# Performance work log

Hardware: AMD Instinct MI355X
Metric: run time of the kernel (lower is better)

Reference implementation:

```python
import jax, jax.numpy as jnp
import numpy as np

B, T, D = 64, 128, 1024
H = 8                       # attention heads
C, S, M = 1000, 5, 10       # num_classes, max_stages, mem_size


def layernorm(x, g, b, eps=1e-5):
    mu = jnp.mean(x, axis=-1, keepdims=True)
    var = jnp.var(x, axis=-1, keepdims=True)
    return (x - mu) / jnp.sqrt(var + eps) * g + b


def linear(x, w, b):
    return x @ w.T + b


def lstm_layer(xin, Wih, Whh, bih, bhh):
    # PyTorch gate order: i, f, g, o
    def step(carry, xt):
        h, c = carry
        gates = xt @ Wih.T + bih + h @ Whh.T + bhh
        i, f, g, o = jnp.split(gates, 4, axis=-1)
        c = jax.nn.sigmoid(f) * c + jax.nn.sigmoid(i) * jnp.tanh(g)
        h = jax.nn.sigmoid(o) * jnp.tanh(c)
        return (h, c), h
    z = jnp.zeros((xin.shape[0], Wih.shape[0] // 4), xin.dtype)
    (hF, _), ys = jax.lax.scan(step, (z, z), jnp.swapaxes(xin, 0, 1))
    return jnp.swapaxes(ys, 0, 1), hF


def setup_inputs() -> dict:
    key = jax.random.key(0)
    ks = iter(jax.random.split(key, 64))

    def w(shape, s=0.02):
        return jax.random.normal(next(ks), shape, jnp.float32) * s

    inp = {
        "x": jax.random.normal(next(ks), (B, T, D), jnp.float32),
        "current_stage": jax.random.randint(next(ks), (B, T), 0, S),
        "class_ids": jax.random.randint(next(ks), (B,), 0, C),
        # stage_encoder: Linear(2,64) -> LN -> ReLU -> Linear(64,D) -> LN
        "enc_w1": w((64, 2)), "enc_b1": jnp.zeros((64,)),
        "enc_g1": jnp.ones((64,)), "enc_bb1": jnp.zeros((64,)),
        "enc_w2": w((D, 64)), "enc_b2": jnp.zeros((D,)),
        "enc_g2": jnp.ones((D,)), "enc_bb2": jnp.zeros((D,)),
        # MultiheadAttention in/out projections
        "qkv_w": w((3 * D, D)), "qkv_b": jnp.zeros((3 * D,)),
        "out_w": w((D, D)), "out_b": jnp.zeros((D,)),
        "norm_g": jnp.ones((D,)), "norm_b": jnp.zeros((D,)),
        # 2-layer LSTM
        "Wih0": w((4 * D, D)), "Whh0": w((4 * D, D)),
        "bih0": jnp.zeros((4 * D,)), "bhh0": jnp.zeros((4 * D,)),
        "Wih1": w((4 * D, D)), "Whh1": w((4 * D, D)),
        "bih1": jnp.zeros((4 * D,)), "bhh1": jnp.zeros((4 * D,)),
        # stage_head
        "head_w1": w((D // 2, D)), "head_b1": jnp.zeros((D // 2,)),
        "head_g": jnp.ones((D // 2,)), "head_bb": jnp.zeros((D // 2,)),
        "head_w2": w((S, D // 2)), "head_b2": jnp.zeros((S,)),
        # GlobalFusion gate
        "gate_w1": w((D, 2 * D)), "gate_b1": jnp.zeros((D,)),
        "gate_w2": w((D, D)), "gate_b2": jnp.zeros((D,)),
        # memory bank buffers
        "memory_features": jnp.zeros((C, S, M, D), jnp.float32),
        "memory_counts": jnp.zeros((C, S), jnp.int32),
    }
    return inp


def reference(x, current_stage, class_ids,
              enc_w1, enc_b1, enc_g1, enc_bb1, enc_w2, enc_b2, enc_g2, enc_bb2,
              qkv_w, qkv_b, out_w, out_b, norm_g, norm_b,
              Wih0, Whh0, bih0, bhh0, Wih1, Whh1, bih1, bhh1,
              head_w1, head_b1, head_g, head_bb, head_w2, head_b2,
              gate_w1, gate_b1, gate_w2, gate_b2,
              memory_features, memory_counts):
    Bx, Tx, Dx = x.shape
    # position + stage encoding
    pos = jnp.broadcast_to(jnp.arange(Tx, dtype=jnp.float32), (Bx, Tx))
    ps = jnp.stack([pos, current_stage.astype(jnp.float32)], axis=-1)  # [B,T,2]
    h = jax.nn.relu(layernorm(linear(ps, enc_w1, enc_b1), enc_g1, enc_bb1))
    pos_emb = layernorm(linear(h, enc_w2, enc_b2), enc_g2, enc_bb2)
    x = x + pos_emb
    # self-attention (torch MultiheadAttention math)
    hd = Dx // H
    qkv = linear(x, qkv_w, qkv_b)
    q, k, v = jnp.split(qkv, 3, axis=-1)
    q = q.reshape(Bx, Tx, H, hd)
    k = k.reshape(Bx, Tx, H, hd)
    v = v.reshape(Bx, Tx, H, hd)
    scores = jnp.einsum('bqhd,bkhd->bhqk', q, k) / jnp.sqrt(jnp.float32(hd))
    attn = jax.nn.softmax(scores, axis=-1)
    o = jnp.einsum('bhqk,bkhd->bqhd', attn, v).reshape(Bx, Tx, Dx)
    attn_out = linear(o, out_w, out_b)
    raw = layernorm(x + attn_out, norm_g, norm_b)  # raw_temporal_feat [B,T,D]
    # 2-layer LSTM (eval mode: no dropout), take last layer final hidden
    y0, _ = lstm_layer(raw, Wih0, Whh0, bih0, bhh0)
    _, pooled = lstm_layer(y0, Wih1, Whh1, bih1, bhh1)  # [B,D]
    raw_mean = jnp.mean(raw, axis=1)
    # gated fusion
    cat = jnp.concatenate([pooled, raw_mean], axis=1)
    g = jax.nn.sigmoid(linear(jax.nn.relu(linear(cat, gate_w1, gate_b1)), gate_w2, gate_b2))
    fused = g * pooled + (1.0 - g) * raw_mean
    # stage head
    logits = linear(jax.nn.relu(layernorm(linear(fused, head_w1, head_b1), head_g, head_bb)),
                    head_w2, head_b2)
    # --- vectorized memory update (no_grad in original) ---
    feats = jax.lax.stop_gradient(raw).reshape(-1, Dx)          # [B*T, D]
    pair = (jnp.repeat(class_ids, Tx) * S + current_stage.reshape(-1)).astype(jnp.int32)
    last = jax.ops.segment_max(jnp.arange(Bx * Tx, dtype=jnp.int32), pair,
                               num_segments=C * S)              # int-min for absent
    present = last >= 0
    newf = feats[jnp.maximum(last, 0)]                          # [C*S, D]
    mem = memory_features.reshape(C * S, M, Dx)
    cnt = memory_counts.reshape(-1)
    full = cnt >= M
    base = jnp.where((present & full)[:, None, None], jnp.roll(mem, -1, axis=1), mem)
    wp = jnp.where(full, M - 1, cnt)
    ar = jnp.arange(C * S)
    cur = base[ar, wp]
    new_mem = base.at[ar, wp].set(jnp.where(present[:, None], newf, cur))
    new_cnt = cnt + (present & ~full).astype(cnt.dtype)
    return (fused, raw, logits,
            new_mem.reshape(C, S, M, Dx), new_cnt.reshape(C, S))
```

## Files before the change

### kernel.cpp

```cpp
#include <hip/hip_runtime.h>
#include <hip/hip_bf16.h>

typedef __bf16 bf16x8 __attribute__((ext_vector_type(8)));
typedef float  f32x4  __attribute__((ext_vector_type(4)));
typedef unsigned long long u64;
using bf16 = __hip_bfloat16;

constexpr int Bv = 64, Tv = 128, Dv = 1024, Hv = 8, HDv = 128;
constexpr int NC = 1000, NS = 5, NM = 10;
constexpr int NT = Bv * Tv;

static __device__ __forceinline__ float sigmoidf_(float x) {
  return 1.f / (1.f + __expf(-x));
}

static __device__ __forceinline__ void gload_lds16(const bf16* g, bf16* l) {
  __builtin_amdgcn_global_load_lds(
      (const __attribute__((address_space(1))) void*)g,
      (__attribute__((address_space(3))) void*)l, 16, 0, 0);
}

static __device__ __forceinline__ float dot8(uint4 w8, const float* c) {
  union { uint4 u; __hip_bfloat162 h[4]; } W; W.u = w8;
  float acc = 0.f;
#pragma unroll
  for (int e = 0; e < 4; ++e) {
    float2 f = __bfloat1622float2(W.h[e]);
    acc += f.x * c[2 * e] + f.y * c[2 * e + 1];
  }
  return acc;
}

__global__ __launch_bounds__(256) void gemm128(
    const bf16* __restrict__ A, const bf16* __restrict__ W,
    const float* __restrict__ bias, bf16* __restrict__ C,
    int M, int N, int K, int transT)
{
  __shared__ bf16 sa[128 * 32];
  __shared__ bf16 sb[128 * 32];
  int wave = threadIdx.x >> 6, lane = threadIdx.x & 63;
  int l15 = lane & 15, lhi = lane >> 4;
  int wr = wave >> 1, wc = wave & 1;
  int row0 = blockIdx.x * 128, col0 = blockIdx.y * 128;
  f32x4 acc[4][4];
#pragma unroll
  for (int m = 0; m < 4; ++m)
#pragma unroll
    for (int n = 0; n < 4; ++n) acc[m][n] = f32x4{0.f, 0.f, 0.f, 0.f};

  int sr = wave * 32 + (lane >> 2);
  int sk = (lane & 3) * 8;
  const bf16* srcA = A + (size_t)(row0 + sr) * K + sk;
  const bf16* srcB = W + (size_t)(col0 + sr) * K + sk;
  bf16* dstA0 = &sa[wave * 1024];
  bf16* dstB0 = &sb[wave * 1024];

  for (int k0 = 0; k0 < K; k0 += 32) {
    __syncthreads();
    gload_lds16(srcA + k0,            dstA0);
    gload_lds16(srcA + 16 * K + k0,   dstA0 + 512);
    gload_lds16(srcB + k0,            dstB0);
    gload_lds16(srcB + 16 * K + k0,   dstB0 + 512);
    __syncthreads();
    bf16x8 af[4], bfr[4];
#pragma unroll
    for (int m = 0; m < 4; ++m)
      af[m] = *reinterpret_cast<const bf16x8*>(&sa[(wr * 64 + m * 16 + l15) * 32 + lhi * 8]);
#pragma unroll
    for (int n = 0; n < 4; ++n)
      bfr[n] = *reinterpret_cast<const bf16x8*>(&sb[(wc * 64 + n * 16 + l15) * 32 + lhi * 8]);
#pragma unroll
    for (int m = 0; m < 4; ++m)
#pragma unroll
      for (int n = 0; n < 4; ++n)
        acc[m][n] = __builtin_amdgcn_mfma_f32_16x16x32_bf16(af[m], bfr[n], acc[m][n], 0, 0, 0);
  }

#pragma unroll
  for (int n = 0; n < 4; ++n) {
    int col = col0 + wc * 64 + n * 16 + l15;
    float bv = bias ? bias[col] : 0.f;
#pragma unroll
    for (int m = 0; m < 4; ++m) {
#pragma unroll
      for (int r = 0; r < 4; ++r) {
        int row = row0 + wr * 64 + m * 16 + lhi * 4 + r;
        int orow = transT ? ((row & (Tv - 1)) * Bv + (row >> 7)) : row;
        C[(size_t)orow * N + col] = __float2bfloat16(acc[m][n][r] + bv);
      }
    }
  }
}

__global__ void convert_all(
    const float* __restrict__ qkv_w, const float* __restrict__ out_w,
    const float* __restrict__ Wih0, const float* __restrict__ Whh0,
    const float* __restrict__ Wih1, const float* __restrict__ Whh1,
    const float* __restrict__ gw1, const float* __restrict__ gw2,
    const float* __restrict__ hw1,
    const float* __restrict__ bih0, const float* __restrict__ bhh0,
    const float* __restrict__ bih1, const float* __restrict__ bhh1,
    bf16* __restrict__ wq16, bf16* __restrict__ wo16,
    bf16* __restrict__ wih0b, bf16* __restrict__ whh0b,
    bf16* __restrict__ wih1b, bf16* __restrict__ whh1b,
    bf16* __restrict__ gw1b, bf16* __restrict__ gw2b, bf16* __restrict__ hw1b,
    float* __restrict__ bsum0, float* __restrict__ bsum1)
{
  long i = (long)blockIdx.x * 256 + threadIdx.x;
  const float* s; bf16* d; long off;
  if (i < 786432)        { s = qkv_w; d = wq16;  off = i; }
  else if (i < 1048576)  { s = out_w; d = wo16;  off = i - 786432; }
  else if (i < 2097152)  { s = Wih0;  d = wih0b; off = i - 1048576; }
  else if (i < 3145728)  { s = Whh0;  d = whh0b; off = i - 2097152; }
  else if (i < 4194304)  { s = Wih1;  d = wih1b; off = i - 3145728; }
  else if (i < 5242880)  { s = Whh1;  d = whh1b; off = i - 4194304; }
  else if (i < 5767168)  { s = gw1;   d = gw1b;  off = i - 5242880; }
  else if (i < 6029312)  { s = gw2;   d = gw2b;  off = i - 5767168; }
  else if (i < 6160384)  { s = hw1;   d = hw1b;  off = i - 6029312; }
  else {
    long k = i - 6160384;
    if (k < 1024) {
      float4 a = ((const float4*)bih0)[k], b = ((const float4*)bhh0)[k];
      ((float4*)bsum0)[k] = make_float4(a.x + b.x, a.y + b.y, a.z + b.z, a.w + b.w);
    } else if (k < 2048) {
      k -= 1024;
      float4 a = ((const float4*)bih1)[k], b = ((const float4*)bhh1)[k];
      ((float4*)bsum1)[k] = make_float4(a.x + b.x, a.y + b.y, a.z + b.z, a.w + b.w);
    }
    return;
  }
  float4 v = ((const float4*)s)[off];
  bf16* o = d + off * 4;
  o[0] = __float2bfloat16(v.x); o[1] = __float2bfloat16(v.y);
  o[2] = __float2bfloat16(v.z); o[3] = __float2bfloat16(v.w);
}

__global__ __launch_bounds__(128) void emb_kernel(
    const float* __restrict__ w1, const float* __restrict__ b1,
    const float* __restrict__ g1, const float* __restrict__ bb1,
    const float* __restrict__ w2, const float* __restrict__ b2,
    const float* __restrict__ g2, const float* __restrict__ bb2,
    float* __restrict__ emb)
{
  int combo = blockIdx.x;
  float tpos = (float)(combo / 5);
  float stg  = (float)(combo % 5);
  int tid = threadIdx.x;
  __shared__ float hb[64];
  __shared__ float rs[4];
  if (tid < 64) {
    float v = w1[tid * 2] * tpos + w1[tid * 2 + 1] * stg + b1[tid];
    float s = v, s2 = v * v;
    for (int off = 32; off; off >>= 1) { s += __shfl_down(s, off); s2 += __shfl_down(s2, off); }
    s = __shfl(s, 0); s2 = __shfl(s2, 0);
    float mu = s / 64.f, var = s2 / 64.f - mu * mu;
    float h = (v - mu) * rsqrtf(var + 1e-5f) * g1[tid] + bb1[tid];
    hb[tid] = fmaxf(h, 0.f);
  }
  __syncthreads();
  float outv[8];
  float s = 0.f, s2 = 0.f;
  int d0 = tid * 8;
#pragma unroll
  for (int o = 0; o < 8; ++o) {
    int d = d0 + o;
    float acc = b2[d];
    const float4* wr = (const float4*)(w2 + (size_t)d * 64);
#pragma unroll
    for (int k4 = 0; k4 < 16; ++k4) {
      float4 w = wr[k4];
      acc += w.x * hb[k4 * 4] + w.y * hb[k4 * 4 + 1] + w.z * hb[k4 * 4 + 2] + w.w * hb[k4 * 4 + 3];
    }
    outv[o] = acc; s += acc; s2 += acc * acc;
  }
  for (int off = 32; off; off >>= 1) { s += __shfl_down(s, off); s2 += __shfl_down(s2, off); }
  int wid = tid >> 6;
  if ((tid & 63) == 0) { rs[wid] = s; rs[2 + wid] = s2; }
  __syncthreads();
  s = rs[0] + rs[1]; s2 = rs[2] + rs[3];
  float mu = s / 1024.f, var = s2 / 1024.f - mu * mu;
  float rstd = rsqrtf(var + 1e-5f);
  float* op = emb + (size_t)combo * Dv + d0;
#pragma unroll
  for (int o = 0; o < 8; ++o) {
    int d = d0 + o;
    op[o] = (outv[o] - mu) * rstd * g2[d] + bb2[d];
  }
}

__global__ __launch_bounds__(256) void addemb_kernel(
    const float* __restrict__ x, const int* __restrict__ stage,
    const float* __restrict__ emb, bf16* __restrict__ xpe)
{
  int tok = blockIdx.x;
  int row = (tok & (Tv - 1)) * NS + stage[tok];
  const float4* xr = (const float4*)(x + (size_t)tok * Dv);
  const float4* er = (const float4*)(emb + (size_t)row * Dv);
  bf16* op = xpe + (size_t)tok * Dv + threadIdx.x * 4;
  float4 xv = xr[threadIdx.x], ev = er[threadIdx.x];
  op[0] = __float2bfloat16(xv.x + ev.x);
  op[1] = __float2bfloat16(xv.y + ev.y);
  op[2] = __float2bfloat16(xv.z + ev.z);
  op[3] = __float2bfloat16(xv.w + ev.w);
}

__global__ __launch_bounds__(256) void attn_kernel(const bf16* __restrict__ qkv,
                                                   bf16* __restrict__ o)
{
  __shared__ bf16 kl[128][128];
  __shared__ bf16 vl[128][128];
  int bh = blockIdx.x;
  int b = bh >> 3, h = bh & 7;
  int tid = threadIdx.x;
  int row = tid >> 1, hf = tid & 1;
  {
    const bf16* ks = qkv + (size_t)(b * Tv + row) * 3072 + Dv + h * HDv + hf * 64;
    const bf16* vs = ks + Dv;
    uint4* dk = (uint4*)&kl[row][hf * 64];
    uint4* dv = (uint4*)&vl[row][hf * 64];
    const uint4* sk = (const uint4*)ks;
    const uint4* sv = (const uint4*)vs;
#pragma unroll
    for (int i = 0; i < 8; ++i) { dk[i] = sk[i]; dv[i] = sv[i]; }
  }
  float qf[64];
  {
    const bf16* qs = qkv + (size_t)(b * Tv + row) * 3072 + h * HDv + hf * 64;
#pragma unroll
    for (int d2 = 0; d2 < 32; ++d2) {
      float2 f = __bfloat1622float2(*(const __hip_bfloat162*)(qs + 2 * d2));
      qf[2 * d2] = f.x; qf[2 * d2 + 1] = f.y;
    }
  }
  __syncthreads();
  float oacc[64];
#pragma unroll
  for (int d = 0; d < 64; ++d) oacc[d] = 0.f;
  float m = -1e30f, l = 0.f;
  const float scale = 0.088388347648318447f;
  for (int j = 0; j < 128; ++j) {
    float part = 0.f;
#pragma unroll
    for (int d2 = 0; d2 < 32; ++d2) {
      float2 kv2 = __bfloat1622float2(*(const __hip_bfloat162*)&kl[j][hf * 64 + 2 * d2]);
      part += qf[2 * d2] * kv2.x + qf[2 * d2 + 1] * kv2.y;
    }
    float sfull = (part + __shfl_xor(part, 1)) * scale;
    float mn = fmaxf(m, sfull);
    float al = __expf(m - mn);
    float p = __expf(sfull - mn);
    l = l * al + p;
#pragma unroll
    for (int d2 = 0; d2 < 32; ++d2) {
      float2 vv = __bfloat1622float2(*(const __hip_bfloat162*)&vl[j][hf * 64 + 2 * d2]);
      oacc[2 * d2]     = oacc[2 * d2] * al + p * vv.x;
      oacc[2 * d2 + 1] = oacc[2 * d2 + 1] * al + p * vv.y;
    }
    m = mn;
  }
  float rl = 1.f / l;
  bf16* od = o + (size_t)(b * Tv + row) * Dv + h * HDv + hf * 64;
#pragma unroll
  for (int d = 0; d < 64; ++d) od[d] = __float2bfloat16(oacc[d] * rl);
}

__global__ __launch_bounds__(256) void residual_ln_kernel(
    const bf16* __restrict__ xpe, const bf16* __restrict__ ao,
    const float* __restrict__ gam, const float* __restrict__ bet,
    float* __restrict__ rawf, bf16* __restrict__ raw16)
{
  int tok = blockIdx.x, tid = threadIdx.x;
  float v[4]; float s = 0.f, s2 = 0.f;
  __shared__ float rs[8];
#pragma unroll
  for (int q = 0; q < 4; ++q) {
    int d = tid + q * 256;
    size_t idx = (size_t)tok * Dv + d;
    float a = __bfloat162float(xpe[idx]) + __bfloat162float(ao[idx]);
    v[q] = a; s += a; s2 += a * a;
  }
  for (int off = 32; off; off >>= 1) { s += __shfl_down(s, off); s2 += __shfl_down(s2, off); }
  int wid = tid >> 6;
  if ((tid & 63) == 0) { rs[wid] = s; rs[4 + wid] = s2; }
  __syncthreads();
  s = rs[0] + rs[1] + rs[2] + rs[3];
  s2 = rs[4] + rs[5] + rs[6] + rs[7];
  float mu = s / 1024.f, var = s2 / 1024.f - mu * mu;
  float rstd = rsqrtf(var + 1e-5f);
#pragma unroll
  for (int q = 0; q < 4; ++q) {
    int d = tid + q * 256;
    size_t idx = (size_t)tok * Dv + d;
    float rv = (v[q] - mu) * rstd * gam[d] + bet[d];
    rawf[idx] = rv;
    raw16[idx] = __float2bfloat16(rv);
  }
}

__global__ __launch_bounds__(512, 1) void lstm_fused(
    const bf16* __restrict__ Whh0, const bf16* __restrict__ Wih1,
    const bf16* __restrict__ Whh1, const bf16* __restrict__ xgT,
    const float* __restrict__ bsum1,
    bf16* h0buf, bf16* h1buf,
    float* __restrict__ pooled, int* flags)
{
  const int bid = blockIdx.x;
  const int xcd = bid & 7, idx = bid >> 3;
  const int j   = xcd * 8 + (idx & 7);
  const int gid = idx >> 3;
  const int u0  = j * 16;
  const int tid = threadIdx.x;
  const int wave = tid >> 6, lane = tid & 63;
  const int g = wave & 3, kh = wave >> 2;
  const int l15 = lane & 15, lhi = lane >> 4;
  const int koff = lhi * 8;

  bf16x8 w0h[16], w1h[16], wh1h[16];
  {
    const size_t rowoff = (size_t)(g * Dv + u0 + l15) * Dv + kh * 512 + koff;
    const bf16* r0 = Whh0 + rowoff;
    const bf16* r1 = Wih1 + rowoff;
    const bf16* r2 = Whh1 + rowoff;
#pragma unroll
    for (int i = 0; i < 16; ++i) {
      w0h[i]  = *reinterpret_cast<const bf16x8*>(r0 + i * 32);
      w1h[i]  = *reinterpret_cast<const bf16x8*>(r1 + i * 32);
      wh1h[i] = *reinterpret_cast<const bf16x8*>(r2 + i * 32);
    }
#pragma unroll
    for (int i = 0; i < 16; ++i) {
      asm volatile("" : "+v"(w0h[i]));
      asm volatile("" : "+v"(w1h[i]));
      asm volatile("" : "+v"(wh1h[i]));
    }
  }
  const float bs1 = bsum1[g * Dv + u0 + l15];

  __shared__ bf16 hA[16 * 2056];
  __shared__ float gl0[2][4][16][16];
  __shared__ float gl1[2][4][16][16];
  __shared__ bf16 hst0[256];
  __shared__ bf16 hst1[256];

  const int bb_t = (tid & 255) >> 4, uu_t = tid & 15;
  float c0 = 0.f, c1 = 0.f;
  int* gflags = flags + gid * 64;

  for (int s = 0; s <= Tv; ++s) {
    float xv[4] = {0.f, 0.f, 0.f, 0.f};
    if (s < Tv && kh == 0) {
      const bf16* xg_t = xgT + (size_t)s * (Bv * 4 * Dv)
                         + (size_t)(gid * 16) * (4 * Dv) + g * Dv + u0 + l15;
#pragma unroll
      for (int r = 0; r < 4; ++r)
        xv[r] = __bfloat162float(xg_t[(size_t)(lhi * 4 + r) * (4 * Dv)]);
    }
    if (s > 0) {
      if (tid < 64) {
        while (true) {
          int v = __hip_atomic_load(gflags + tid, __ATOMIC_RELAXED, __HIP_MEMORY_SCOPE_AGENT);
          if (__all(v >= s)) break;
          __builtin_amdgcn_s_sleep(1);
        }
      }
      __syncthreads();
      {
        const u64* s0 = (const u64*)h0buf + (size_t)(((s - 1) & 1) * 4 + gid) * 4096;
        u64* dA = (u64*)hA;
#pragma unroll
        for (int it = 0; it < 8; ++it) {
          int id = it * 512 + tid;
          int jc = id >> 6, r = id & 63, bb = r >> 2, uq = r & 3;
          u64 v = __hip_atomic_load(s0 + id, __ATOMIC_RELAXED, __HIP_MEMORY_SCOPE_AGENT);
          dA[bb * 514 + jc * 4 + uq] = v;
        }
        if (s >= 2) {
          const u64* s1 = (const u64*)h1buf + (size_t)(((s - 2) & 1) * 4 + gid) * 4096;
#pragma unroll
          for (int it = 0; it < 8; ++it) {
            int id = it * 512 + tid;
            int jc = id >> 6, r = id & 63, bb = r >> 2, uq = r & 3;
            u64 v = __hip_atomic_load(s1 + id, __ATOMIC_RELAXED, __HIP_MEMORY_SCOPE_AGENT);
            dA[bb * 514 + 256 + jc * 4 + uq] = v;
          }
        }
      }
      __syncthreads();
    }

    if (s < Tv) {
      f32x4 acc = f32x4{0.f, 0.f, 0.f, 0.f};
      if (s > 0) {
#pragma unroll
        for (int i = 0; i < 16; ++i) {
          bf16x8 a = *reinterpret_cast<const bf16x8*>(&hA[l15 * 2056 + kh * 512 + i * 32 + koff]);
          acc = __builtin_amdgcn_mfma_f32_16x16x32_bf16(a, w0h[i], acc, 0, 0, 0);
        }
      }
#pragma unroll
      for (int r = 0; r < 4; ++r)
        gl0[kh][g][lhi * 4 + r][l15] = acc[r] + xv[r];
    }
    if (s > 0) {
      f32x4 acc = f32x4{0.f, 0.f, 0.f, 0.f};
#pragma unroll
      for (int i = 0; i < 16; ++i) {
        bf16x8 a = *reinterpret_cast<const bf16x8*>(&hA[l15 * 2056 + kh * 512 + i * 32 + koff]);
        acc = __builtin_amdgcn_mfma_f32_16x16x32_bf16(a, w1h[i], acc, 0, 0, 0);
      }
      if (s >= 2) {
#pragma unroll
        for (int i = 0; i < 16; ++i) {
          bf16x8 a = *reinterpret_cast<const bf16x8*>(&hA[l15 * 2056 + 1024 + kh * 512 + i * 32 + koff]);
          acc = __builtin_amdgcn_mfma_f32_16x16x32_bf16(a, wh1h[i], acc, 0, 0, 0);
        }
      }
#pragma unroll
      for (int r = 0; r < 4; ++r)
        gl1[kh][g][lhi * 4 + r][l15] = acc[r] + (kh == 0 ? bs1 : 0.f);
    }
    __syncthreads();
    if (tid < 256) {
      if (s < Tv) {
        float gi = gl0[0][0][bb_t][uu_t] + gl0[1][0][bb_t][uu_t];
        float gf = gl0[0][1][bb_t][uu_t] + gl0[1][1][bb_t][uu_t];
        float gc = gl0[0][2][bb_t][uu_t] + gl0[1][2][bb_t][uu_t];
        float go = gl0[0][3][bb_t][uu_t] + gl0[1][3][bb_t][uu_t];
        float cn = sigmoidf_(gf) * c0 + sigmoidf_(gi) * tanhf(gc);
        float hn = sigmoidf_(go) * tanhf(cn);
        c0 = cn;
        hst0[bb_t * 16 + uu_t] = __float2bfloat16(hn);
      }
      if (s > 0) {
        float gi = gl1[0][0][bb_t][uu_t] + gl1[1][0][bb_t][uu_t];
        float gf = gl1[0][1][bb_t][uu_t] + gl1[1][1][bb_t][uu_t];
        float gc = gl1[0][2][bb_t][uu_t] + gl1[1][2][bb_t][uu_t];
        float go = gl1[0][3][bb_t][uu_t] + gl1[1][3][bb_t][uu_t];
        float cn = sigmoidf_(gf) * c1 + sigmoidf_(gi) * tanhf(gc);
        float hn = sigmoidf_(go) * tanhf(cn);
        c1 = cn;
        hst1[bb_t * 16 + uu_t] = __float2bfloat16(hn);
        if (s == Tv) pooled[(gid * 16 + bb_t) * Dv + u0 + uu_t] = hn;
      }
    }
    __syncthreads();
    if (s < Tv && tid < 64) {
      u64* dst = (u64*)h0buf + (size_t)((s & 1) * 4 + gid) * 4096 + j * 64 + tid;
      __hip_atomic_store(dst, ((u64*)hst0)[tid], __ATOMIC_RELAXED, __HIP_MEMORY_SCOPE_AGENT);
    }
    if (s > 0 && tid >= 64 && tid < 128) {
      int q = tid - 64;
      u64* dst = (u64*)h1buf + (size_t)(((s - 1) & 1) * 4 + gid) * 4096 + j * 64 + q;
      __hip_atomic_store(dst, ((u64*)hst1)[q], __ATOMIC_RELAXED, __HIP_MEMORY_SCOPE_AGENT);
    }
    if (s < Tv) {
      asm volatile("s_waitcnt vmcnt(0)" ::: "memory");
      __syncthreads();
      if (tid == 0)
        __hip_atomic_store(gflags + j, s + 1, __ATOMIC_RELAXED, __HIP_MEMORY_SCOPE_AGENT);
    }
  }
}

__global__ void rawmean_kernel(const float* __restrict__ raw, float* __restrict__ out)
{
  int i = blockIdx.x * 256 + threadIdx.x;
  int b = i >> 10, d = i & 1023;
  const float* r = raw + (size_t)b * Tv * Dv + d;
  float s = 0.f;
  for (int t = 0; t < Tv; ++t) s += r[(size_t)t * Dv];
  out[i] = s * (1.f / Tv);
}

__global__ __launch_bounds__(256) void gatehead_kernel(
    const float* __restrict__ pooled, const float* __restrict__ rawmean,
    const bf16* __restrict__ gw1b, const float* __restrict__ gb1,
    const bf16* __restrict__ gw2b, const float* __restrict__ gb2,
    const bf16* __restrict__ hw1b, const float* __restrict__ hb1,
    const float* __restrict__ hg, const float* __restrict__ hbb,
    const float* __restrict__ hw2, const float* __restrict__ hb2,
    float* __restrict__ fused_out, float* __restrict__ logits)
{
  int b = blockIdx.x, tid = threadIdx.x;
  __shared__ float cat[2048];
  __shared__ float g1v[1024];
  __shared__ float fl[1024];
  __shared__ float h1[512];
  __shared__ float rs[8];
  for (int k = tid; k < 1024; k += 256) {
    cat[k] = pooled[b * 1024 + k];
    cat[1024 + k] = rawmean[b * 1024 + k];
  }
  __syncthreads();
  for (int jj = 0; jj < 4; ++jj) {
    int j = tid + jj * 256;
    float acc = gb1[j];
    const uint4* wr = (const uint4*)(gw1b + (size_t)j * 2048);
    for (int ku = 0; ku < 256; ++ku) acc += dot8(wr[ku], &cat[ku * 8]);
    g1v[j] = fmaxf(acc, 0.f);
  }
  __syncthreads();
  for (int jj = 0; jj < 4; ++jj) {
    int j = tid + jj * 256;
    float acc = gb2[j];
    const uint4* wr = (const uint4*)(gw2b + (size_t)j * 1024);
    for (int ku = 0; ku < 128; ++ku) acc += dot8(wr[ku], &g1v[ku * 8]);
    float gv = sigmoidf_(acc);
    float f = gv * cat[j] + (1.f - gv) * cat[1024 + j];
    fused_out[b * 1024 + j] = f;
    fl[j] = f;
  }
  __syncthreads();
  float v0, v1;
  {
    float acc = hb1[tid];
    const uint4* wr = (const uint4*)(hw1b + (size_t)tid * 1024);
    for (int ku = 0; ku < 128; ++ku) acc += dot8(wr[ku], &fl[ku * 8]);
    v0 = acc;
    acc = hb1[tid + 256];
    wr = (const uint4*)(hw1b + (size_t)(tid + 256) * 1024);
    for (int ku = 0; ku < 128; ++ku) acc += dot8(wr[ku], &fl[ku * 8]);
    v1 = acc;
  }
  float s = v0 + v1, s2 = v0 * v0 + v1 * v1;
  for (int off = 32; off; off >>= 1) { s += __shfl_down(s, off); s2 += __shfl_down(s2, off); }
  int wid = tid >> 6;
  if ((tid & 63) == 0) { rs[wid] = s; rs[4 + wid] = s2; }
  __syncthreads();
  s = rs[0] + rs[1] + rs[2] + rs[3];
  s2 = rs[4] + rs[5] + rs[6] + rs[7];
  float mu = s / 512.f, var = s2 / 512.f - mu * mu;
  float rstd = rsqrtf(var + 1e-5f);
  h1[tid]       = fmaxf((v0 - mu) * rstd * hg[tid] + hbb[tid], 0.f);
  h1[tid + 256] = fmaxf((v1 - mu) * rstd * hg[tid + 256] + hbb[tid + 256], 0.f);
  __syncthreads();
  if (tid < 5) {
    float acc = hb2[tid];
    for (int k = 0; k < 512; ++k) acc += h1[k] * hw2[tid * 512 + k];
    logits[b * 5 + tid] = acc;
  }
}

__global__ void scatter_last_kernel(const int* __restrict__ cls,
                                    const int* __restrict__ stage, int* __restrict__ last)
{
  int i = blockIdx.x * 256 + threadIdx.x;
  if (i < NT) {
    int b = i >> 7;
    int p = cls[b] * NS + stage[i];
    atomicMax(&last[p], i);
  }
}

__global__ __launch_bounds__(256) void mem_update_kernel(
    const float* __restrict__ mem_in, const float* __restrict__ raw,
    const int* __restrict__ cnt_in, const int* __restrict__ last,
    float* __restrict__ mem_out, float* __restrict__ cnt_out)
{
  int p = blockIdx.x;
  int cnt = cnt_in[p];
  int li = last[p];
  bool present = li >= 0;
  bool full = cnt >= NM;
  int wp = full ? NM - 1 : cnt;
  const float* newf = raw + (size_t)(li < 0 ? 0 : li) * Dv;
  const float* src = mem_in + (size_t)p * NM * Dv;
  float* dst = mem_out + (size_t)p * NM * Dv;
  for (int idx = threadIdx.x; idx < NM * Dv / 4; idx += 256) {
    int m = idx >> 8;
    int dq = idx & 255;
    float4 v;
    if (present && full) {
      v = (m < NM - 1) ? *(const float4*)(src + (size_t)(m + 1) * Dv + dq * 4)
                       : *(const float4*)(newf + dq * 4);
    } else if (present) {
      v = (m == wp) ? *(const float4*)(newf + dq * 4)
                    : *(const float4*)(src + (size_t)m * Dv + dq * 4);
    } else {
      v = *(const float4*)(src + (size_t)m * Dv + dq * 4);
    }
    *(float4*)(dst + (size_t)m * Dv + dq * 4) = v;
  }
  if (threadIdx.x == 0)
    cnt_out[p] = (float)(cnt + ((present && !full) ? 1 : 0));
}

extern "C" void kernel_launch(void* const* d_in, const int* in_sizes, int n_in,
                              void* d_out, int out_size, void* d_ws, size_t ws_size,
                              hipStream_t stream)
{
  (void)in_sizes; (void)n_in; (void)out_size; (void)ws_size;
  const float* x       = (const float*)d_in[0];
  const int* stage     = (const int*)d_in[1];
  const int* cls       = (const int*)d_in[2];
  const float* enc_w1  = (const float*)d_in[3];
  const float* enc_b1  = (const float*)d_in[4];
  const float* enc_g1  = (const float*)d_in[5];
  const float* enc_bb1 = (const float*)d_in[6];
  const float* enc_w2  = (const float*)d_in[7];
  const float* enc_b2  = (const float*)d_in[8];
  const float* enc_g2  = (const float*)d_in[9];
  const float* enc_bb2 = (const float*)d_in[10];
  const float* qkv_w   = (const float*)d_in[11];
  const float* qkv_b   = (const float*)d_in[12];
  const float* out_w   = (const float*)d_in[13];
  const float* out_b   = (const float*)d_in[14];
  const float* norm_g  = (const float*)d_in[15];
  const float* norm_b  = (const float*)d_in[16];
  const float* Wih0    = (const float*)d_in[17];
  const float* Whh0    = (const float*)d_in[18];
  const float* bih0    = (const float*)d_in[19];
  const float* bhh0    = (const float*)d_in[20];
  const float* Wih1    = (const float*)d_in[21];
  const float* Whh1    = (const float*)d_in[22];
  const float* bih1    = (const float*)d_in[23];
  const float* bhh1    = (const float*)d_in[24];
  const float* head_w1 = (const float*)d_in[25];
  const float* head_b1 = (const float*)d_in[26];
  const float* head_g  = (const float*)d_in[27];
  const float* head_bb = (const float*)d_in[28];
  const float* head_w2 = (const float*)d_in[29];
  const float* head_b2 = (const float*)d_in[30];
  const float* gate_w1 = (const float*)d_in[31];
  const float* gate_b1 = (const float*)d_in[32];
  const float* gate_w2 = (const float*)d_in[33];
  const float* gate_b2 = (const float*)d_in[34];
  const float* mem_in  = (const float*)d_in[35];
  const int* cnt_in    = (const int*)d_in[36];

  float* out = (float*)d_out;
  float* out_fused  = out;
  float* out_raw    = out + 65536;
  float* out_logits = out + 8454144;
  float* out_mem    = out + 8454464;
  float* out_cnt    = out + 59654464;

  char* wsb = (char*)d_ws;
  auto alloc = [&](size_t bytes) { char* p = wsb; wsb += (bytes + 255) & ~(size_t)255; return p; };
  bf16* wq16   = (bf16*)alloc((size_t)3072 * 1024 * 2);
  bf16* wo16   = (bf16*)alloc((size_t)1024 * 1024 * 2);
  bf16* wih0b  = (bf16*)alloc((size_t)4096 * 1024 * 2);
  bf16* whh0b  = (bf16*)alloc((size_t)4096 * 1024 * 2);
  bf16* wih1b  = (bf16*)alloc((size_t)4096 * 1024 * 2);
  bf16* whh1b  = (bf16*)alloc((size_t)4096 * 1024 * 2);
  bf16* gw1b   = (bf16*)alloc((size_t)1024 * 2048 * 2);
  bf16* gw2b   = (bf16*)alloc((size_t)1024 * 1024 * 2);
  bf16* hw1b   = (bf16*)alloc((size_t)512 * 1024 * 2);
  float* bsum0 = (float*)alloc(4096 * 4);
  float* bsum1 = (float*)alloc(4096 * 4);
  bf16* h0buf  = (bf16*)alloc((size_t)2 * 4 * 16384 * 2);
  bf16* h1buf  = (bf16*)alloc((size_t)2 * 4 * 16384 * 2);
  float* pooled  = (float*)alloc(65536 * 4);
  float* rawmean = (float*)alloc(65536 * 4);
  int* last      = (int*)alloc(5000 * 4);
  int* flags     = (int*)alloc(1024);

  char* orb = (char*)out_mem;
  bf16* qkv16 = (bf16*)(orb + 0);
  bf16* xgT   = (bf16*)(orb + 67108864);
  bf16* xpe16 = (bf16*)(orb + 134217728);
  bf16* o16   = (bf16*)(orb + 150994944);
  bf16* ao16  = (bf16*)(orb + 167772160);
  bf16* raw16 = (bf16*)(orb + 184549376);
  float* embf = (float*)(orb + 201326592);

  convert_all<<<24072, 256, 0, stream>>>(qkv_w, out_w, Wih0, Whh0, Wih1, Whh1,
                                         gate_w1, gate_w2, head_w1,
                                         bih0, bhh0, bih1, bhh1,
                                         wq16, wo16, wih0b, whh0b, wih1b, whh1b,
                                         gw1b, gw2b, hw1b, bsum0, bsum1);

  emb_kernel<<<Tv * NS, 128, 0, stream>>>(enc_w1, enc_b1, enc_g1, enc_bb1,
                                          enc_w2, enc_b2, enc_g2, enc_bb2, embf);
  addemb_kernel<<<NT, 256, 0, stream>>>(x, stage, embf, xpe16);

  gemm128<<<dim3(NT / 128, 3072 / 128), 256, 0, stream>>>(xpe16, wq16, qkv_b, qkv16,
                                                          NT, 3072, Dv, 0);

  attn_kernel<<<Bv * Hv, 256, 0, stream>>>(qkv16, o16);

  gemm128<<<dim3(NT / 128, 1024 / 128), 256, 0, stream>>>(o16, wo16, out_b, ao16,
                                                          NT, Dv, Dv, 0);

  residual_ln_kernel<<<NT, 256, 0, stream>>>(xpe16, ao16, norm_g, norm_b, out_raw, raw16);

  gemm128<<<dim3(NT / 128, 4096 / 128), 256, 0, stream>>>(raw16, wih0b, bsum0, xgT,
                                                          NT, 4096, Dv, 1);
  hipMemsetAsync(flags, 0, 1024, stream);
  lstm_fused<<<256, 512, 0, stream>>>(whh0b, wih1b, whh1b, xgT, bsum1,
                                      h0buf, h1buf, pooled, flags);

  rawmean_kernel<<<256, 256, 0, stream>>>(out_raw, rawmean);
  gatehead_kernel<<<Bv, 256, 0, stream>>>(pooled, rawmean,
                                          gw1b, gate_b1, gw2b, gate_b2,
                                          hw1b, head_b1, head_g, head_bb,
                                          head_w2, head_b2, out_fused, out_logits);

  hipMemsetAsync(last, 0xFF, 5000 * 4, stream);
  scatter_last_kernel<<<32, 256, 0, stream>>>(cls, stage, last);
  mem_update_kernel<<<NC * NS, 256, 0, stream>>>(mem_in, out_raw, cnt_in, last, out_mem, out_cnt);
}
```

Baseline: 1.855 ms.

## Swizzle GEMM block order across XCDs and trim LSTM step synchronisation

The GEMM launches switch to a 1D grid whose block index is remapped so that consecutive workgroups landing on the same XCD cover neighbouring tiles, which is meant to improve L2 reuse of A and W tiles. In the LSTM step, both hidden-state publishes now come from the first wave, which lets the barrier before the flag store be dropped and shortens the per-step critical path. The independent memsets and the scatter kernel move to the start of the stream. The swizzle assumes the grid size is divisible by 8. Dropping the barrier relies on the first wave's vmcnt wait alone to order the hidden-state stores before the flag is published.

```diff
diff --git a/kernel.cpp b/kernel.cpp
--- a/kernel.cpp
+++ b/kernel.cpp
@@ -34,14 +34,18 @@
 __global__ __launch_bounds__(256) void gemm128(
     const bf16* __restrict__ A, const bf16* __restrict__ W,
     const float* __restrict__ bias, bf16* __restrict__ C,
-    int M, int N, int K, int transT)
+    int M, int N, int K, int transT, int gridX)
 {
   __shared__ bf16 sa[128 * 32];
   __shared__ bf16 sb[128 * 32];
+  int nwg = gridDim.x;
+  int q = nwg >> 3;
+  int swz = (blockIdx.x & 7) * q + (blockIdx.x >> 3);
+  int bx = swz % gridX, by = swz / gridX;
   int wave = threadIdx.x >> 6, lane = threadIdx.x & 63;
   int l15 = lane & 15, lhi = lane >> 4;
   int wr = wave >> 1, wc = wave & 1;
-  int row0 = blockIdx.x * 128, col0 = blockIdx.y * 128;
+  int row0 = bx * 128, col0 = by * 128;
   f32x4 acc[4][4];
 #pragma unroll
   for (int m = 0; m < 4; ++m)
@@ -444,18 +448,14 @@
       }
     }
     __syncthreads();
-    if (s < Tv && tid < 64) {
-      u64* dst = (u64*)h0buf + (size_t)((s & 1) * 4 + gid) * 4096 + j * 64 + tid;
-      __hip_atomic_store(dst, ((u64*)hst0)[tid], __ATOMIC_RELAXED, __HIP_MEMORY_SCOPE_AGENT);
-    }
-    if (s > 0 && tid >= 64 && tid < 128) {
-      int q = tid - 64;
-      u64* dst = (u64*)h1buf + (size_t)(((s - 1) & 1) * 4 + gid) * 4096 + j * 64 + q;
-      __hip_atomic_store(dst, ((u64*)hst1)[q], __ATOMIC_RELAXED, __HIP_MEMORY_SCOPE_AGENT);
-    }
-    if (s < Tv) {
+    if (tid < 64 && s < Tv) {
+      u64* dst0 = (u64*)h0buf + (size_t)((s & 1) * 4 + gid) * 4096 + j * 64 + tid;
+      __hip_atomic_store(dst0, ((u64*)hst0)[tid], __ATOMIC_RELAXED, __HIP_MEMORY_SCOPE_AGENT);
+      if (s > 0) {
+        u64* dst1 = (u64*)h1buf + (size_t)(((s - 1) & 1) * 4 + gid) * 4096 + j * 64 + tid;
+        __hip_atomic_store(dst1, ((u64*)hst1)[tid], __ATOMIC_RELAXED, __HIP_MEMORY_SCOPE_AGENT);
+      }
       asm volatile("s_waitcnt vmcnt(0)" ::: "memory");
-      __syncthreads();
       if (tid == 0)
         __hip_atomic_store(gflags + j, s + 1, __ATOMIC_RELAXED, __HIP_MEMORY_SCOPE_AGENT);
     }
@@ -664,6 +664,10 @@
   bf16* raw16 = (bf16*)(orb + 184549376);
   float* embf = (float*)(orb + 201326592);
 
+  hipMemsetAsync(flags, 0, 1024, stream);
+  hipMemsetAsync(last, 0xFF, 5000 * 4, stream);
+  scatter_last_kernel<<<32, 256, 0, stream>>>(cls, stage, last);
+
   convert_all<<<24072, 256, 0, stream>>>(qkv_w, out_w, Wih0, Whh0, Wih1, Whh1,
                                          gate_w1, gate_w2, head_w1,
                                          bih0, bhh0, bih1, bhh1,
@@ -674,19 +678,18 @@
                                           enc_w2, enc_b2, enc_g2, enc_bb2, embf);
   addemb_kernel<<<NT, 256, 0, stream>>>(x, stage, embf, xpe16);
 
-  gemm128<<<dim3(NT / 128, 3072 / 128), 256, 0, stream>>>(xpe16, wq16, qkv_b, qkv16,
-                                                          NT, 3072, Dv, 0);
+  gemm128<<<(NT / 128) * (3072 / 128), 256, 0, stream>>>(xpe16, wq16, qkv_b, qkv16,
+                                                         NT, 3072, Dv, 0, NT / 128);
 
   attn_kernel<<<Bv * Hv, 256, 0, stream>>>(qkv16, o16);
 
-  gemm128<<<dim3(NT / 128, 1024 / 128), 256, 0, stream>>>(o16, wo16, out_b, ao16,
-                                                          NT, Dv, Dv, 0);
+  gemm128<<<(NT / 128) * (1024 / 128), 256, 0, stream>>>(o16, wo16, out_b, ao16,
+                                                         NT, Dv, Dv, 0, NT / 128);
 
   residual_ln_kernel<<<NT, 256, 0, stream>>>(xpe16, ao16, norm_g, norm_b, out_raw, raw16);
 
-  gemm128<<<dim3(NT / 128, 4096 / 128), 256, 0, stream>>>(raw16, wih0b, bsum0, xgT,
-                                                          NT, 4096, Dv, 1);
-  hipMemsetAsync(flags, 0, 1024, stream);
+  gemm128<<<(NT / 128) * (4096 / 128), 256, 0, stream>>>(raw16, wih0b, bsum0, xgT,
+                                                         NT, 4096, Dv, 1, NT / 128);
   lstm_fused<<<256, 512, 0, stream>>>(whh0b, wih1b, whh1b, xgT, bsum1,
                                       h0buf, h1buf, pooled, flags);
 
@@ -696,7 +699,5 @@
                                           hw1b, head_b1, head_g, head_bb,
                                           head_w2, head_b2, out_fused, out_logits);
 
-  hipMemsetAsync(last, 0xFF, 5000 * 4, stream);
-  scatter_last_kernel<<<32, 256, 0, stream>>>(cls, stage, last);
   mem_update_kernel<<<NC * NS, 256, 0, stream>>>(mem_in, out_raw, cnt_in, last, out_mem, out_cnt);
 }
```

Result: no change. 1.883 ms (+1.5%).
